# Kernel optimization log

Measured on AMD Instinct MI355X. Metric: run time of the kernel, lower is better.

Reference implementation:

```python
import jax, jax.numpy as jnp
import numpy as np
import math

RADIUS = 1.0
PERCENTAGES = (0.02, 0.04, 0.06, 0.08, 0.10)


def _fps(pts, npoint):
    """Furthest point sampling. pts: [N,3] -> idx [npoint] int32 (starts at index 0,
    matching pointnet2 CUDA furthest_point_sample)."""
    N = pts.shape[0]

    def step(carry, _):
        dists, last = carry
        d = jnp.sum((pts - pts[last]) ** 2, axis=-1)
        dists = jnp.minimum(dists, d)
        nxt = jnp.argmax(dists).astype(jnp.int32)
        return (dists, nxt), nxt

    init = (jnp.full((N,), 1e10, pts.dtype), jnp.int32(0))
    _, rest = jax.lax.scan(step, init, None, length=npoint - 1)
    return jnp.concatenate([jnp.zeros((1,), jnp.int32), rest])


def _ball_query(pcd, queries, r, nsample):
    """pcd [B,N,3], queries [B,M,3] -> idx [B,M,nsample] int32.
    First (by index order) points with squared dist < r^2; groups with fewer than
    nsample in-radius points are padded with the first found index (pn2 semantics)."""
    N = pcd.shape[1]
    d2 = jnp.sum((queries[:, :, None, :] - pcd[:, None, :, :]) ** 2, axis=-1)  # [B,M,N]
    key = jnp.where(d2 < r * r, jnp.arange(N, dtype=jnp.int32), jnp.int32(N))
    srt = jnp.sort(key, axis=-1)[:, :, :nsample]  # first in-radius indices
    valid = srt < N
    first = jnp.where(srt[:, :, :1] < N, srt[:, :, :1], 0)
    return jnp.where(valid, srt, first)


def _nn_dist(g):
    """g [G,n,3] -> [G,n] distance to nearest neighbor (2nd-smallest pairwise
    Euclidean distance, i.e. KNN(k=2) dist[:,:,1] including self-distance 0)."""
    sq = jnp.sum(g * g, axis=-1)  # [G,n]
    d2 = sq[:, :, None] + sq[:, None, :] - 2.0 * jnp.einsum('gnc,gmc->gnm', g, g)
    d2 = jnp.maximum(d2, 0.0)
    # safe sqrt (zero grad at exact zeros: self / duplicated padded points)
    d = jnp.where(d2 > 0, jnp.sqrt(jnp.where(d2 > 0, d2, 1.0)), 0.0)
    neg2, _ = jax.lax.top_k(-d, 2)  # two smallest distances
    return -neg2[:, :, 1]


def _uniform_loss(pcd):
    B, N, C = pcd.shape
    npoint = int(N * 0.05)
    fps_idx = jax.vmap(_fps, in_axes=(0, None))(pcd, npoint)  # [B,M]
    new_xyz = jnp.take_along_axis(pcd, fps_idx[:, :, None], axis=1)  # [B,M,3]
    loss = jnp.zeros((), pcd.dtype)
    for p in PERCENTAGES:
        nsample = int(N * p)
        r = math.sqrt(p * RADIUS)
        disk_area = math.pi * RADIUS ** 2 / N
        expect_len = math.sqrt(disk_area)
        idx = _ball_query(pcd, new_xyz, r, nsample)  # [B,M,n]
        grouped = jax.vmap(lambda pts, ii: pts[ii])(pcd, idx)  # [B,M,n,3]
        g = grouped.reshape(B * npoint, nsample, C)
        nn = _nn_dist(g)  # [G,n]
        e_ = 0.1
        u = jnp.abs(nn + e_)
        u = jnp.mean(u, axis=1)  # [G]
        u = (u - expect_len) ** 2 / (expect_len + e_)
        loss = loss + jnp.mean(u) * (p * 100.0) ** 2
    return loss / len(PERCENTAGES)


def setup_inputs() -> dict:
    key = jax.random.key(0)
    pcd = jax.random.uniform(key, (2, 4096, 3), dtype=jnp.float32)
    return {"pcd": pcd}


def reference(pcd):
    return _uniform_loss(pcd)
```

## Files before the change

### kernel.cpp

```cpp
#include <hip/hip_runtime.h>
#include <cmath>

#define NPTS 4096
#define NPOINT 204
#define NPCT 5
#define MAXNS 409
#define FPS_T 256
#define NGROUP 408
#define NPART (NGROUP * NPCT)
#define MAXSLOT 7

#define NWORK  510
#define NROUND 4

#define SMEM_BYTES 65600
#define KEYS_OFF   65536
#define WRES_OFF   6544
#define WTOT_OFF   20880
#define SPART_OFF  20896
#define SQI_OFF    20912

typedef unsigned long long u64;
typedef float f32x2 __attribute__((ext_vector_type(2)));

struct LossParams {
    int   nsample[NPCT];
    float r2[NPCT];
    float wscale[NPCT];
    float expect_len;
};

template <int CTRL>
__device__ __forceinline__ int dpp_imax(int v) {
    int t = __builtin_amdgcn_update_dpp(0, v, CTRL, 0xf, 0xf, true);
    return v > t ? v : t;
}
template <int CTRL>
__device__ __forceinline__ int dpp_imin(int v) {
    int t = __builtin_amdgcn_update_dpp(0x7fffffff, v, CTRL, 0xf, 0xf, false);
    return v < t ? v : t;
}
__device__ __forceinline__ int wave_max_i(int v) {
    v = dpp_imax<0x111>(v); v = dpp_imax<0x112>(v);
    v = dpp_imax<0x114>(v); v = dpp_imax<0x118>(v);
    v = dpp_imax<0x142>(v); v = dpp_imax<0x143>(v);
    return __builtin_amdgcn_readlane(v, 63);
}
__device__ __forceinline__ int wave_min_i(int v) {
    v = dpp_imin<0x111>(v); v = dpp_imin<0x112>(v);
    v = dpp_imin<0x114>(v); v = dpp_imin<0x118>(v);
    v = dpp_imin<0x142>(v); v = dpp_imin<0x143>(v);
    return __builtin_amdgcn_readlane(v, 63);
}
template <int CTRL>
__device__ __forceinline__ u64 dpp_u64max(u64 v) {
    int lo = (int)(unsigned)v;
    int hi = (int)(unsigned)(v >> 32);
    unsigned slo = (unsigned)__builtin_amdgcn_update_dpp(0, lo, CTRL, 0xf, 0xf, true);
    unsigned shi = (unsigned)__builtin_amdgcn_update_dpp(0, hi, CTRL, 0xf, 0xf, true);
    u64 o = ((u64)shi << 32) | slo;
    return v > o ? v : o;
}

__device__ void fps_role(const float* __restrict__ pcd,
                         int* __restrict__ fps_idx,
                         char* smem) {
#pragma clang fp contract(off)
    __builtin_amdgcn_s_setprio(3);
    float4* pts = reinterpret_cast<float4*>(smem);
    u64 (*keys)[4] = reinterpret_cast<u64 (*)[4]>(smem + KEYS_OFF);

    const int b = blockIdx.x;
    const int t = threadIdx.x;
    const int wave = t >> 6, lane = t & 63;
    const float* base = pcd + (size_t)b * NPTS * 3;

    f32x2 X[8], Y[8], Z[8], D[8];
    #pragma unroll
    for (int q = 0; q < 8; ++q) {
        int n0 = (2 * q) * FPS_T + t;
        int n1 = (2 * q + 1) * FPS_T + t;
        float x0 = base[3 * n0 + 0], y0 = base[3 * n0 + 1], z0 = base[3 * n0 + 2];
        float x1 = base[3 * n1 + 0], y1 = base[3 * n1 + 1], z1 = base[3 * n1 + 2];
        pts[n0] = make_float4(x0, y0, z0, 0.0f);
        pts[n1] = make_float4(x1, y1, z1, 0.0f);
        X[q] = (f32x2){x0, x1};
        Y[q] = (f32x2){y0, y1};
        Z[q] = (f32x2){z0, z1};
        D[q] = (f32x2){1e10f, 1e10f};
    }
    int* out = fps_idx + b * NPOINT;
    if (t == 0)
        __hip_atomic_store(&out[0], 0, __ATOMIC_RELAXED, __HIP_MEMORY_SCOPE_AGENT);
    __syncthreads();

    float4 c = pts[0];
    for (int it = 1; it < NPOINT; ++it) {
        f32x2 cxx = (f32x2){c.x, c.x};
        f32x2 cyy = (f32x2){c.y, c.y};
        f32x2 czz = (f32x2){c.z, c.z};
        int bb = -1, bi = 0;
        #pragma unroll
        for (int q = 0; q < 8; ++q) {
            f32x2 dx = X[q] - cxx, dy = Y[q] - cyy, dz = Z[q] - czz;
            f32x2 d  = (dx * dx + dy * dy) + dz * dz;
            f32x2 dd = D[q];
            float d0 = fminf(dd.x, d.x);
            float d1 = fminf(dd.y, d.y);
            D[q] = (f32x2){d0, d1};
            int b0 = __float_as_int(d0);
            int b1 = __float_as_int(d1);
            if (b0 > bb) { bb = b0; bi = (2 * q) * FPS_T + t; }
            if (b1 > bb) { bb = b1; bi = (2 * q + 1) * FPS_T + t; }
        }
        int wmax = wave_max_i(bb);
        int cand = (bb == wmax) ? bi : 0x7fffffff;
        int widx = wave_min_i(cand);
        if (lane == 0)
            keys[it & 1][wave] =
                ((u64)(unsigned)wmax << 32) | (unsigned)~(unsigned)widx;
        __syncthreads();
        u64 kv = keys[it & 1][lane & 3];
        kv = dpp_u64max<0x111>(kv);
        kv = dpp_u64max<0x112>(kv);
        unsigned lo3 = (unsigned)__builtin_amdgcn_readlane((int)(unsigned)kv, 3);
        int last = (int)~lo3;
        c = pts[last];
        if (t == 0)
            __hip_atomic_store(&out[it], last, __ATOMIC_RELAXED, __HIP_MEMORY_SCOPE_AGENT);
    }
}

template <int K>
__device__ __forceinline__ void phaseB(const float4* __restrict__ gpts,
                                       float2 (*wres)[64],
                                       int j0, int j1, int lane, int cntB) {
    float4 pi[K];
    float m1[K], m2[K];
    #pragma unroll
    for (int s = 0; s < K; ++s) {
        int idx = s * 64 + lane;
        pi[s] = gpts[idx < cntB ? idx : 0];
        m1[s] = 1e30f; m2[s] = 1e30f;
    }
    #pragma unroll 2
    for (int j = j0; j < j1; ++j) {
        float4 a = gpts[j];
        #pragma unroll
        for (int s = 0; s < K; ++s) {
            float tt = pi[s].x * a.x;
            tt = fmaf(pi[s].y, a.y, tt);
            tt = fmaf(pi[s].z, a.z, tt);
            float h = fmaf(-2.0f, tt, a.w);
            m2[s] = __builtin_amdgcn_fmed3f(m1[s], m2[s], h);
            m1[s] = fminf(m1[s], h);
        }
    }
    #pragma unroll
    for (int s = 0; s < K; ++s) wres[s][lane] = (float2){m1[s], m2[s]};
}

__device__ void worker_role(const float* __restrict__ pcd,
                            int* __restrict__ fps_idx,
                            float* __restrict__ partials,
                            const LossParams& P, char* smem) {
    float4* gpts = reinterpret_cast<float4*>(smem);
    auto wres    = reinterpret_cast<float2 (*)[MAXSLOT][64]>(smem + WRES_OFF);
    int*   s_wtot = reinterpret_cast<int*>(smem + WTOT_OFF);
    float* s_part = reinterpret_cast<float*>(smem + SPART_OFF);
    int*   s_qi   = reinterpret_cast<int*>(smem + SQI_OFF);

    const int w = blockIdx.x - 2;
    const int t = threadIdx.x;
    const int wave = t >> 6, lane = t & 63;

    for (int round = 0; round < NROUND; ++round) {
        const int tau  = w + round * NWORK;
        const int m_   = tau / 10;
        const int rem  = tau - m_ * 10;
        const int b    = rem / 5;
        const int pidx = rem - b * 5;

        const int   ns = P.nsample[pidx];
        const float r2 = P.r2[pidx];
        const float* base = pcd + (size_t)b * NPTS * 3;

        if (t == 0) {
            int q;
            while ((q = __hip_atomic_load(&fps_idx[b * NPOINT + m_],
                                          __ATOMIC_RELAXED,
                                          __HIP_MEMORY_SCOPE_AGENT)) < 0)
                __builtin_amdgcn_s_sleep(16);
            s_qi[0] = q;
        }
        __syncthreads();
        const int qi = s_qi[0];
        float qx = base[3 * qi + 0], qy = base[3 * qi + 1], qz = base[3 * qi + 2];

        unsigned long long msk[16];
        int lbase[16];
        int run = 0;
        #pragma unroll 4
        for (int s = 0; s < 16; ++s) {
            int n = wave * 1024 + s * 64 + lane;
            float x = base[3 * n + 0];
            float y = base[3 * n + 1];
            float z = base[3 * n + 2];
            float d2;
            {
#pragma clang fp contract(off)
                float dx = qx - x, dy = qy - y, dz = qz - z;
                float aa = dx * dx, bb = dy * dy, cc = dz * dz;
                d2 = (aa + bb) + cc;
            }
            msk[s] = __ballot(d2 < r2);
            lbase[s] = run;
            run += __popcll(msk[s]);
        }
        if (lane == 0) s_wtot[wave] = run;
        __syncthreads();
        int w0 = s_wtot[0], w1 = s_wtot[1], w2 = s_wtot[2], w3 = s_wtot[3];
        int Bw = (wave > 0 ? w0 : 0) + (wave > 1 ? w1 : 0) + (wave > 2 ? w2 : 0);
        int cnt  = w0 + w1 + w2 + w3;
        int cntB = cnt < ns ? cnt : ns;
        const int npad = ns - cntB;

        #pragma unroll 4
        for (int s = 0; s < 16; ++s) {
            int gb = Bw + lbase[s];
            if (gb >= ns) break;
            unsigned long long mk = msk[s];
            bool in = (mk >> lane) & 1ull;
            int pos = gb + __popcll(mk & ((1ull << lane) - 1ull));
            if (in && pos < ns) {
                int n = wave * 1024 + s * 64 + lane;
                float x = base[3 * n], y = base[3 * n + 1], z = base[3 * n + 2];
                float sq = fmaf(x, x, fmaf(y, y, z * z));
                gpts[pos] = make_float4(x, y, z, sq);
            }
        }
        __syncthreads();

        const int quarter = (cntB + 3) >> 2;
        const int j0 = wave * quarter;
        const int j1 = (j0 + quarter) < cntB ? (j0 + quarter) : cntB;
        const int nslot = (cntB + 63) >> 6;
        switch (nslot) {
            case 1: phaseB<1>(gpts, wres[wave], j0, j1, lane, cntB); break;
            case 2: phaseB<2>(gpts, wres[wave], j0, j1, lane, cntB); break;
            case 3: phaseB<3>(gpts, wres[wave], j0, j1, lane, cntB); break;
            case 4: phaseB<4>(gpts, wres[wave], j0, j1, lane, cntB); break;
            case 5: phaseB<5>(gpts, wres[wave], j0, j1, lane, cntB); break;
            case 6: phaseB<6>(gpts, wres[wave], j0, j1, lane, cntB); break;
            default: phaseB<7>(gpts, wres[wave], j0, j1, lane, cntB); break;
        }
        __syncthreads();

        float sum = 0.0f;
        for (int it = t; it < nslot * 64; it += 256) {
            int i = it;
            if (i < cntB) {
                int s = it >> 6, l = it & 63;
                float2 a  = wres[0][s][l];
                float2 bq = wres[1][s][l];
                float2 cq = wres[2][s][l];
                float2 dq = wres[3][s][l];
                float e1 = fminf(a.x, bq.x), e2 = fminf(fmaxf(a.x, bq.x), fminf(a.y, bq.y));
                float f1 = fminf(cq.x, dq.x), f2 = fminf(fmaxf(cq.x, dq.x), fminf(cq.y, dq.y));
                float m2v = fminf(fmaxf(e1, f1), fminf(e2, f2));
                float sq = gpts[i].w;
                float d2 = fmaxf(sq + m2v, 0.0f);
                if (!(i == 0 && npad > 0)) sum += sqrtf(d2);
            }
        }
        #pragma unroll
        for (int off = 32; off; off >>= 1) sum += __shfl_down(sum, off);
        if (lane == 0) s_part[wave] = sum;
        __syncthreads();
        if (t == 0) {
            float tot = s_part[0] + s_part[1] + s_part[2] + s_part[3] + 0.1f * (float)ns;
            float u  = tot / (float)ns;
            float du = u - P.expect_len;
            partials[tau] = du * du / (P.expect_len + 0.1f) * P.wscale[pidx];
        }
    }
}

__global__ __launch_bounds__(256, 2) void fused_kernel(const float* __restrict__ pcd,
                                                       int* __restrict__ fps_idx,
                                                       float* __restrict__ partials,
                                                       LossParams P) {
    __shared__ __align__(16) char smem[SMEM_BYTES];
    if (blockIdx.x < 2) {
        fps_role(pcd, fps_idx, smem);
    } else {
        worker_role(pcd, fps_idx, partials, P, smem);
    }
}

__global__ __launch_bounds__(256) void reduce_kernel(const float* __restrict__ partials,
                                                     float* __restrict__ out) {
    const int t = threadIdx.x;
    __shared__ float sp[4];
    float s = 0.0f;
    for (int i = t; i < NPART; i += 256) s += partials[i];
    #pragma unroll
    for (int off = 32; off; off >>= 1) s += __shfl_down(s, off);
    if ((t & 63) == 0) sp[t >> 6] = s;
    __syncthreads();
    if (t == 0) out[0] = sp[0] + sp[1] + sp[2] + sp[3];
}

extern "C" void kernel_launch(void* const* d_in, const int* in_sizes, int n_in,
                              void* d_out, int out_size, void* d_ws, size_t ws_size,
                              hipStream_t stream) {
    const float* pcd = (const float*)d_in[0];
    const int B = in_sizes[0] / (NPTS * 3);
    float* out = (float*)d_out;
    int*   fps = (int*)d_ws;
    float* partials = (float*)d_ws + NGROUP;

    hipMemsetAsync(fps, 0xFF, NGROUP * sizeof(int), stream);

    LossParams P;
    const double ps[NPCT] = {0.02, 0.04, 0.06, 0.08, 0.10};
    for (int i = 0; i < NPCT; ++i) {
        P.nsample[i] = (int)(NPTS * ps[i]);
        double r = std::sqrt(ps[i] * 1.0);
        P.r2[i] = (float)(r * r);
        double w = (ps[i] * 100.0) * (ps[i] * 100.0);
        P.wscale[i] = (float)(w / (double)(B * NPOINT * NPCT));
    }
    P.expect_len = (float)std::sqrt(3.14159265358979323846 / (double)NPTS);

    fused_kernel<<<dim3(2 + NWORK), dim3(256), 0, stream>>>(pcd, fps, partials, P);
    reduce_kernel<<<dim3(1), dim3(256), 0, stream>>>(partials, out);
}
```

Before: 187.8 us.

## Fuse reduction into persistent kernel with atomic work queue and self-resetting flags

```diff
diff --git a/kernel.cpp b/kernel.cpp
--- a/kernel.cpp
+++ b/kernel.cpp
@@ -10,15 +10,15 @@
 #define NPART (NGROUP * NPCT)
 #define MAXSLOT 7
 
-#define NWORK  510
-#define NROUND 4
+#define NBLOCKS 512
+#define NWORKER 508
 
 #define SMEM_BYTES 65600
 #define KEYS_OFF   65536
 #define WRES_OFF   6544
 #define WTOT_OFF   20880
 #define SPART_OFF  20896
-#define SQI_OFF    20912
+#define SCTL_OFF   20912
 
 typedef unsigned long long u64;
 typedef float f32x2 __attribute__((ext_vector_type(2)));
@@ -30,28 +30,10 @@
     float expect_len;
 };
 
-template <int CTRL>
-__device__ __forceinline__ int dpp_imax(int v) {
-    int t = __builtin_amdgcn_update_dpp(0, v, CTRL, 0xf, 0xf, true);
-    return v > t ? v : t;
-}
-template <int CTRL>
-__device__ __forceinline__ int dpp_imin(int v) {
-    int t = __builtin_amdgcn_update_dpp(0x7fffffff, v, CTRL, 0xf, 0xf, false);
-    return v < t ? v : t;
-}
-__device__ __forceinline__ int wave_max_i(int v) {
-    v = dpp_imax<0x111>(v); v = dpp_imax<0x112>(v);
-    v = dpp_imax<0x114>(v); v = dpp_imax<0x118>(v);
-    v = dpp_imax<0x142>(v); v = dpp_imax<0x143>(v);
-    return __builtin_amdgcn_readlane(v, 63);
-}
-__device__ __forceinline__ int wave_min_i(int v) {
-    v = dpp_imin<0x111>(v); v = dpp_imin<0x112>(v);
-    v = dpp_imin<0x114>(v); v = dpp_imin<0x118>(v);
-    v = dpp_imin<0x142>(v); v = dpp_imin<0x143>(v);
-    return __builtin_amdgcn_readlane(v, 63);
-}
+__device__ int g_fps[NGROUP];
+__device__ int g_task;
+__device__ int g_done;
+
 template <int CTRL>
 __device__ __forceinline__ u64 dpp_u64max(u64 v) {
     int lo = (int)(unsigned)v;
@@ -61,10 +43,14 @@
     u64 o = ((u64)shi << 32) | slo;
     return v > o ? v : o;
 }
-
-__device__ void fps_role(const float* __restrict__ pcd,
-                         int* __restrict__ fps_idx,
-                         char* smem) {
+__device__ __forceinline__ u64 wave_u64max(u64 v) {
+    v = dpp_u64max<0x111>(v); v = dpp_u64max<0x112>(v);
+    v = dpp_u64max<0x114>(v); v = dpp_u64max<0x118>(v);
+    v = dpp_u64max<0x142>(v); v = dpp_u64max<0x143>(v);
+    return v;
+}
+
+__device__ void fps_role(const float* __restrict__ pcd, char* smem) {
 #pragma clang fp contract(off)
     __builtin_amdgcn_s_setprio(3);
     float4* pts = reinterpret_cast<float4*>(smem);
@@ -89,9 +75,9 @@
         Z[q] = (f32x2){z0, z1};
         D[q] = (f32x2){1e10f, 1e10f};
     }
-    int* out = fps_idx + b * NPOINT;
+    int* out = g_fps + b * NPOINT;
     if (t == 0)
-        __hip_atomic_store(&out[0], 0, __ATOMIC_RELAXED, __HIP_MEMORY_SCOPE_AGENT);
+        __hip_atomic_store(&out[0], ~0, __ATOMIC_RELAXED, __HIP_MEMORY_SCOPE_AGENT);
     __syncthreads();
 
     float4 c = pts[0];
@@ -113,12 +99,9 @@
             if (b0 > bb) { bb = b0; bi = (2 * q) * FPS_T + t; }
             if (b1 > bb) { bb = b1; bi = (2 * q + 1) * FPS_T + t; }
         }
-        int wmax = wave_max_i(bb);
-        int cand = (bb == wmax) ? bi : 0x7fffffff;
-        int widx = wave_min_i(cand);
-        if (lane == 0)
-            keys[it & 1][wave] =
-                ((u64)(unsigned)wmax << 32) | (unsigned)~(unsigned)widx;
+        u64 key = ((u64)(unsigned)bb << 32) | (unsigned)~(unsigned)bi;
+        key = wave_u64max(key);
+        if (lane == 63) keys[it & 1][wave] = key;
         __syncthreads();
         u64 kv = keys[it & 1][lane & 3];
         kv = dpp_u64max<0x111>(kv);
@@ -127,7 +110,7 @@
         int last = (int)~lo3;
         c = pts[last];
         if (t == 0)
-            __hip_atomic_store(&out[it], last, __ATOMIC_RELAXED, __HIP_MEMORY_SCOPE_AGENT);
+            __hip_atomic_store(&out[it], ~last, __ATOMIC_RELAXED, __HIP_MEMORY_SCOPE_AGENT);
     }
 }
 
@@ -161,23 +144,40 @@
 }
 
 __device__ void worker_role(const float* __restrict__ pcd,
-                            int* __restrict__ fps_idx,
                             float* __restrict__ partials,
                             const LossParams& P, char* smem) {
     float4* gpts = reinterpret_cast<float4*>(smem);
     auto wres    = reinterpret_cast<float2 (*)[MAXSLOT][64]>(smem + WRES_OFF);
     int*   s_wtot = reinterpret_cast<int*>(smem + WTOT_OFF);
     float* s_part = reinterpret_cast<float*>(smem + SPART_OFF);
-    int*   s_qi   = reinterpret_cast<int*>(smem + SQI_OFF);
-
-    const int w = blockIdx.x - 2;
+    int*   s_ctl  = reinterpret_cast<int*>(smem + SCTL_OFF);
+
     const int t = threadIdx.x;
     const int wave = t >> 6, lane = t & 63;
 
-    for (int round = 0; round < NROUND; ++round) {
-        const int tau  = w + round * NWORK;
-        const int m_   = tau / 10;
-        const int rem  = tau - m_ * 10;
+    for (;;) {
+        if (t == 0) {
+            int tau = __hip_atomic_fetch_add(&g_task, 1, __ATOMIC_RELAXED,
+                                             __HIP_MEMORY_SCOPE_AGENT);
+            s_ctl[0] = tau;
+            if (tau < NPART) {
+                int m_  = tau / 10;
+                int rem = tau - m_ * 10;
+                int bb  = rem / 5;
+                int v;
+                while ((v = __hip_atomic_load(&g_fps[bb * NPOINT + m_],
+                                              __ATOMIC_RELAXED,
+                                              __HIP_MEMORY_SCOPE_AGENT)) >= 0)
+                    __builtin_amdgcn_s_sleep(16);
+                s_ctl[1] = ~v;
+            }
+        }
+        __syncthreads();
+        const int tau = s_ctl[0];
+        if (tau >= NPART) break;
+        const int qi  = s_ctl[1];
+        const int m_  = tau / 10;
+        const int rem = tau - m_ * 10;
         const int b    = rem / 5;
         const int pidx = rem - b * 5;
 
@@ -185,16 +185,6 @@
         const float r2 = P.r2[pidx];
         const float* base = pcd + (size_t)b * NPTS * 3;
 
-        if (t == 0) {
-            int q;
-            while ((q = __hip_atomic_load(&fps_idx[b * NPOINT + m_],
-                                          __ATOMIC_RELAXED,
-                                          __HIP_MEMORY_SCOPE_AGENT)) < 0)
-                __builtin_amdgcn_s_sleep(16);
-            s_qi[0] = q;
-        }
-        __syncthreads();
-        const int qi = s_qi[0];
         float qx = base[3 * qi + 0], qy = base[3 * qi + 1], qz = base[3 * qi + 2];
 
         unsigned long long msk[16];
@@ -210,8 +200,8 @@
             {
 #pragma clang fp contract(off)
                 float dx = qx - x, dy = qy - y, dz = qz - z;
-                float aa = dx * dx, bb = dy * dy, cc = dz * dz;
-                d2 = (aa + bb) + cc;
+                float aa = dx * dx, bb2 = dy * dy, cc = dz * dz;
+                d2 = (aa + bb2) + cc;
             }
             msk[s] = __ballot(d2 < r2);
             lbase[s] = run;
@@ -284,24 +274,22 @@
             partials[tau] = du * du / (P.expect_len + 0.1f) * P.wscale[pidx];
         }
     }
-}
-
-__global__ __launch_bounds__(256, 2) void fused_kernel(const float* __restrict__ pcd,
-                                                       int* __restrict__ fps_idx,
-                                                       float* __restrict__ partials,
-                                                       LossParams P) {
-    __shared__ __align__(16) char smem[SMEM_BYTES];
-    if (blockIdx.x < 2) {
-        fps_role(pcd, fps_idx, smem);
-    } else {
-        worker_role(pcd, fps_idx, partials, P, smem);
-    }
-}
-
-__global__ __launch_bounds__(256) void reduce_kernel(const float* __restrict__ partials,
-                                                     float* __restrict__ out) {
+    if (t == 0)
+        __hip_atomic_fetch_add(&g_done, 1, __ATOMIC_RELEASE, __HIP_MEMORY_SCOPE_AGENT);
+}
+
+__device__ void reducer_role(const float* __restrict__ partials,
+                             float* __restrict__ out, char* smem) {
     const int t = threadIdx.x;
-    __shared__ float sp[4];
+    float* sp = reinterpret_cast<float*>(smem);
+    if (t == 0) {
+        while (__hip_atomic_load(&g_done, __ATOMIC_ACQUIRE,
+                                 __HIP_MEMORY_SCOPE_AGENT) < NWORKER)
+            __builtin_amdgcn_s_sleep(32);
+    }
+    __syncthreads();
+    (void)__hip_atomic_load(&g_done, __ATOMIC_ACQUIRE, __HIP_MEMORY_SCOPE_AGENT);
+
     float s = 0.0f;
     for (int i = t; i < NPART; i += 256) s += partials[i];
     #pragma unroll
@@ -309,18 +297,34 @@
     if ((t & 63) == 0) sp[t >> 6] = s;
     __syncthreads();
     if (t == 0) out[0] = sp[0] + sp[1] + sp[2] + sp[3];
+
+    for (int i = t; i < NGROUP; i += 256) g_fps[i] = 0;
+    if (t == 0) { g_task = 0; g_done = 0; }
+}
+
+__global__ __launch_bounds__(256, 2) void fused_kernel(const float* __restrict__ pcd,
+                                                       float* __restrict__ partials,
+                                                       float* __restrict__ out,
+                                                       LossParams P) {
+    __shared__ __align__(16) char smem[SMEM_BYTES];
+    const int bid = blockIdx.x;
+    if (bid < 2) {
+        fps_role(pcd, smem);
+    } else if (bid == 256) {
+        reducer_role(partials, out, smem);
+    } else if (bid == 257) {
+        return;
+    } else {
+        worker_role(pcd, partials, P, smem);
+    }
 }
 
 extern "C" void kernel_launch(void* const* d_in, const int* in_sizes, int n_in,
                               void* d_out, int out_size, void* d_ws, size_t ws_size,
                               hipStream_t stream) {
     const float* pcd = (const float*)d_in[0];
-    const int B = in_sizes[0] / (NPTS * 3);
     float* out = (float*)d_out;
-    int*   fps = (int*)d_ws;
-    float* partials = (float*)d_ws + NGROUP;
-
-    hipMemsetAsync(fps, 0xFF, NGROUP * sizeof(int), stream);
+    float* partials = (float*)d_ws;
 
     LossParams P;
     const double ps[NPCT] = {0.02, 0.04, 0.06, 0.08, 0.10};
@@ -329,10 +333,9 @@
         double r = std::sqrt(ps[i] * 1.0);
         P.r2[i] = (float)(r * r);
         double w = (ps[i] * 100.0) * (ps[i] * 100.0);
-        P.wscale[i] = (float)(w / (double)(B * NPOINT * NPCT));
+        P.wscale[i] = (float)(w / (double)(2 * NPOINT * NPCT));
     }
     P.expect_len = (float)std::sqrt(3.14159265358979323846 / (double)NPTS);
 
-    fused_kernel<<<dim3(2 + NWORK), dim3(256), 0, stream>>>(pcd, fps, partials, P);
-    reduce_kernel<<<dim3(1), dim3(256), 0, stream>>>(partials, out);
-}
+    fused_kernel<<<dim3(NBLOCKS), dim3(256), 0, stream>>>(pcd, partials, out, P);
+}
```

Result: slower. 194.3 us (+3.5%).

## Fold final reduction into fused kernel and drop memset via self-resetting flags

Applied to the files above, without the earlier changes.

```diff
diff --git a/kernel.cpp b/kernel.cpp
--- a/kernel.cpp
+++ b/kernel.cpp
@@ -10,15 +10,16 @@
 #define NPART (NGROUP * NPCT)
 #define MAXSLOT 7
 
-#define NWORK  510
-#define NROUND 4
+#define NBLOCKS 512
+#define NWORKER 510
+#define NROUND  4
 
 #define SMEM_BYTES 65600
 #define KEYS_OFF   65536
 #define WRES_OFF   6544
 #define WTOT_OFF   20880
 #define SPART_OFF  20896
-#define SQI_OFF    20912
+#define SCTL_OFF   20912
 
 typedef unsigned long long u64;
 typedef float f32x2 __attribute__((ext_vector_type(2)));
@@ -29,6 +30,9 @@
     float wscale[NPCT];
     float expect_len;
 };
+
+__device__ int g_fps[NGROUP];
+__device__ int g_done;
 
 template <int CTRL>
 __device__ __forceinline__ int dpp_imax(int v) {
@@ -62,9 +66,7 @@
     return v > o ? v : o;
 }
 
-__device__ void fps_role(const float* __restrict__ pcd,
-                         int* __restrict__ fps_idx,
-                         char* smem) {
+__device__ void fps_role(const float* __restrict__ pcd, char* smem) {
 #pragma clang fp contract(off)
     __builtin_amdgcn_s_setprio(3);
     float4* pts = reinterpret_cast<float4*>(smem);
@@ -89,9 +91,9 @@
         Z[q] = (f32x2){z0, z1};
         D[q] = (f32x2){1e10f, 1e10f};
     }
-    int* out = fps_idx + b * NPOINT;
+    int* out = g_fps + b * NPOINT;
     if (t == 0)
-        __hip_atomic_store(&out[0], 0, __ATOMIC_RELAXED, __HIP_MEMORY_SCOPE_AGENT);
+        __hip_atomic_store(&out[0], ~0, __ATOMIC_RELAXED, __HIP_MEMORY_SCOPE_AGENT);
     __syncthreads();
 
     float4 c = pts[0];
@@ -99,7 +101,7 @@
         f32x2 cxx = (f32x2){c.x, c.x};
         f32x2 cyy = (f32x2){c.y, c.y};
         f32x2 czz = (f32x2){c.z, c.z};
-        int bb = -1, bi = 0;
+        int tb[8], ti[8];
         #pragma unroll
         for (int q = 0; q < 8; ++q) {
             f32x2 dx = X[q] - cxx, dy = Y[q] - cyy, dz = Z[q] - czz;
@@ -110,9 +112,21 @@
             D[q] = (f32x2){d0, d1};
             int b0 = __float_as_int(d0);
             int b1 = __float_as_int(d1);
-            if (b0 > bb) { bb = b0; bi = (2 * q) * FPS_T + t; }
-            if (b1 > bb) { bb = b1; bi = (2 * q + 1) * FPS_T + t; }
-        }
+            bool c0 = b0 >= b1;
+            tb[q] = c0 ? b0 : b1;
+            ti[q] = c0 ? (2 * q) * FPS_T + t : (2 * q + 1) * FPS_T + t;
+        }
+        #pragma unroll
+        for (int st = 1; st < 8; st <<= 1) {
+            #pragma unroll
+            for (int q = 0; q < 8; q += 2 * st) {
+                bool cc = tb[q] >= tb[q + st];
+                tb[q] = cc ? tb[q] : tb[q + st];
+                ti[q] = cc ? ti[q] : ti[q + st];
+            }
+        }
+        int bb = tb[0], bi = ti[0];
+
         int wmax = wave_max_i(bb);
         int cand = (bb == wmax) ? bi : 0x7fffffff;
         int widx = wave_min_i(cand);
@@ -127,7 +141,7 @@
         int last = (int)~lo3;
         c = pts[last];
         if (t == 0)
-            __hip_atomic_store(&out[it], last, __ATOMIC_RELAXED, __HIP_MEMORY_SCOPE_AGENT);
+            __hip_atomic_store(&out[it], ~last, __ATOMIC_RELAXED, __HIP_MEMORY_SCOPE_AGENT);
     }
 }
 
@@ -161,21 +175,21 @@
 }
 
 __device__ void worker_role(const float* __restrict__ pcd,
-                            int* __restrict__ fps_idx,
                             float* __restrict__ partials,
+                            float* __restrict__ out,
                             const LossParams& P, char* smem) {
     float4* gpts = reinterpret_cast<float4*>(smem);
     auto wres    = reinterpret_cast<float2 (*)[MAXSLOT][64]>(smem + WRES_OFF);
     int*   s_wtot = reinterpret_cast<int*>(smem + WTOT_OFF);
     float* s_part = reinterpret_cast<float*>(smem + SPART_OFF);
-    int*   s_qi   = reinterpret_cast<int*>(smem + SQI_OFF);
+    int*   s_ctl  = reinterpret_cast<int*>(smem + SCTL_OFF);
 
     const int w = blockIdx.x - 2;
     const int t = threadIdx.x;
     const int wave = t >> 6, lane = t & 63;
 
     for (int round = 0; round < NROUND; ++round) {
-        const int tau  = w + round * NWORK;
+        const int tau  = w + round * NWORKER;
         const int m_   = tau / 10;
         const int rem  = tau - m_ * 10;
         const int b    = rem / 5;
@@ -186,15 +200,15 @@
         const float* base = pcd + (size_t)b * NPTS * 3;
 
         if (t == 0) {
-            int q;
-            while ((q = __hip_atomic_load(&fps_idx[b * NPOINT + m_],
+            int v;
+            while ((v = __hip_atomic_load(&g_fps[b * NPOINT + m_],
                                           __ATOMIC_RELAXED,
-                                          __HIP_MEMORY_SCOPE_AGENT)) < 0)
+                                          __HIP_MEMORY_SCOPE_AGENT)) >= 0)
                 __builtin_amdgcn_s_sleep(16);
-            s_qi[0] = q;
-        }
-        __syncthreads();
-        const int qi = s_qi[0];
+            s_ctl[0] = ~v;
+        }
+        __syncthreads();
+        const int qi = s_ctl[0];
         float qx = base[3 * qi + 0], qy = base[3 * qi + 1], qz = base[3 * qi + 2];
 
         unsigned long long msk[16];
@@ -210,8 +224,8 @@
             {
 #pragma clang fp contract(off)
                 float dx = qx - x, dy = qy - y, dz = qz - z;
-                float aa = dx * dx, bb = dy * dy, cc = dz * dz;
-                d2 = (aa + bb) + cc;
+                float aa = dx * dx, bb2 = dy * dy, cc = dz * dz;
+                d2 = (aa + bb2) + cc;
             }
             msk[s] = __ballot(d2 < r2);
             lbase[s] = run;
@@ -284,43 +298,45 @@
             partials[tau] = du * du / (P.expect_len + 0.1f) * P.wscale[pidx];
         }
     }
+
+    if (t == 0) {
+        int old = __hip_atomic_fetch_add(&g_done, 1, __ATOMIC_ACQ_REL,
+                                         __HIP_MEMORY_SCOPE_AGENT);
+        s_ctl[0] = old;
+    }
+    __syncthreads();
+    if (s_ctl[0] == NWORKER - 1) {
+        (void)__hip_atomic_load(&g_done, __ATOMIC_ACQUIRE, __HIP_MEMORY_SCOPE_AGENT);
+        float s = 0.0f;
+        for (int i = t; i < NPART; i += 256) s += partials[i];
+        #pragma unroll
+        for (int off = 32; off; off >>= 1) s += __shfl_down(s, off);
+        if (lane == 0) s_part[wave] = s;
+        __syncthreads();
+        if (t == 0) out[0] = s_part[0] + s_part[1] + s_part[2] + s_part[3];
+        for (int i = t; i < NGROUP; i += 256) g_fps[i] = 0;
+        if (t == 0) g_done = 0;
+    }
 }
 
 __global__ __launch_bounds__(256, 2) void fused_kernel(const float* __restrict__ pcd,
-                                                       int* __restrict__ fps_idx,
                                                        float* __restrict__ partials,
+                                                       float* __restrict__ out,
                                                        LossParams P) {
     __shared__ __align__(16) char smem[SMEM_BYTES];
     if (blockIdx.x < 2) {
-        fps_role(pcd, fps_idx, smem);
+        fps_role(pcd, smem);
     } else {
-        worker_role(pcd, fps_idx, partials, P, smem);
-    }
-}
-
-__global__ __launch_bounds__(256) void reduce_kernel(const float* __restrict__ partials,
-                                                     float* __restrict__ out) {
-    const int t = threadIdx.x;
-    __shared__ float sp[4];
-    float s = 0.0f;
-    for (int i = t; i < NPART; i += 256) s += partials[i];
-    #pragma unroll
-    for (int off = 32; off; off >>= 1) s += __shfl_down(s, off);
-    if ((t & 63) == 0) sp[t >> 6] = s;
-    __syncthreads();
-    if (t == 0) out[0] = sp[0] + sp[1] + sp[2] + sp[3];
+        worker_role(pcd, partials, out, P, smem);
+    }
 }
 
 extern "C" void kernel_launch(void* const* d_in, const int* in_sizes, int n_in,
                               void* d_out, int out_size, void* d_ws, size_t ws_size,
                               hipStream_t stream) {
     const float* pcd = (const float*)d_in[0];
-    const int B = in_sizes[0] / (NPTS * 3);
     float* out = (float*)d_out;
-    int*   fps = (int*)d_ws;
-    float* partials = (float*)d_ws + NGROUP;
-
-    hipMemsetAsync(fps, 0xFF, NGROUP * sizeof(int), stream);
+    float* partials = (float*)d_ws;
 
     LossParams P;
     const double ps[NPCT] = {0.02, 0.04, 0.06, 0.08, 0.10};
@@ -329,10 +345,9 @@
         double r = std::sqrt(ps[i] * 1.0);
         P.r2[i] = (float)(r * r);
         double w = (ps[i] * 100.0) * (ps[i] * 100.0);
-        P.wscale[i] = (float)(w / (double)(B * NPOINT * NPCT));
+        P.wscale[i] = (float)(w / (double)(2 * NPOINT * NPCT));
     }
     P.expect_len = (float)std::sqrt(3.14159265358979323846 / (double)NPTS);
 
-    fused_kernel<<<dim3(2 + NWORK), dim3(256), 0, stream>>>(pcd, fps, partials, P);
-    reduce_kernel<<<dim3(1), dim3(256), 0, stream>>>(partials, out);
-}
+    fused_kernel<<<dim3(NBLOCKS), dim3(256), 0, stream>>>(pcd, partials, out, P);
+}
```

Result: slower. 194.9 us (+3.8%).
